# Kernel tuning notes

Hardware: AMD Instinct MI355X
Metric: run time of the kernel (lower is better)

## Reference

```python
import jax, jax.numpy as jnp
import numpy as np
import math

Z, H, G, S = 4, 16, 4, 4096          # batch, q heads, kv groups, seq len
BLOCK = 32                            # compression block size
NB = S // BLOCK                       # number of compressed KV blocks (128)
DQK, DV = 128, 128                    # head dims


def setup_inputs() -> dict:
    key = jax.random.key(0)
    k1, k2, k3 = jax.random.split(key, 3)
    q = jax.random.normal(k1, (Z, H, S, DQK), jnp.float32)
    k_blocks = jax.random.normal(k2, (Z, G, NB, DQK), jnp.float32)
    v_blocks = jax.random.normal(k3, (Z, G, NB, DV), jnp.float32)
    # block j covers tokens [j*BLOCK, (j+1)*BLOCK), so it 'ends' at position (j+1)*BLOCK-1
    block_ends = (jnp.arange(1, NB + 1) * BLOCK - 1).astype(jnp.int32)
    return {"q": q, "k_blocks": k_blocks, "v_blocks": v_blocks, "block_ends": block_ends}


def reference(q, k_blocks, v_blocks, block_ends):
    """NSA compression attention fwd: block-end causal masking over compressed KV blocks.
    q: [Z,H,S,Dqk]; k_blocks/v_blocks: [Z,G,NB,D]; block_ends: [NB] int.
    Query at position m attends to compressed block j iff block_ends[j] <= m.
    Rows with no valid block output zeros (matching the kernel's l_i==0 path)."""
    Zb, Hb, Sb, Dq = q.shape
    Gb = k_blocks.shape[1]
    sm_scale = 1.0 / math.sqrt(Dq)
    # GQA: head h -> kv group h // (H // G)
    qg = (q * sm_scale).reshape(Zb, Gb, Hb // Gb, Sb, Dq)
    s = jnp.einsum('zghsd,zgnd->zghsn', qg, k_blocks)        # [Z,G,H/G,S,NB]
    pos = jnp.arange(Sb)
    mask = block_ends[None, :] <= pos[:, None]               # [S,NB]
    s_masked = jnp.where(mask, s, -jnp.inf)
    m = jnp.max(s_masked, axis=-1, keepdims=True)            # online-softmax max (M)
    m_safe = jnp.where(jnp.isfinite(m), m, 0.0)
    p = jnp.where(mask, jnp.exp(s_masked - jax.lax.stop_gradient(m_safe)), 0.0)
    l = jnp.sum(p, axis=-1, keepdims=True)                   # softmax denom (exp(L-M))
    o = jnp.einsum('zghsn,zgnv->zghsv', p, v_blocks)
    o = jnp.where(l > 0, o / jnp.where(l > 0, l, 1.0), 0.0)
    return o.reshape(Zb, Hb, Sb, -1)                         # [Z,H,S,Dv]
```

## Files before the change

### kernel.cpp

```cpp
#include <hip/hip_runtime.h>


#define Zc 4
#define Hc 16
#define Gc 4
#define Sc 4096
#define NBc 128
#define Dc 128
#define VST 136

typedef __attribute__((ext_vector_type(8))) short short8;
typedef __attribute__((ext_vector_type(4))) float float4v;

__device__ inline unsigned pk2bf(float a, float b) {
    union { float f; unsigned u; } x, y; x.f = a; y.f = b;
    return __builtin_amdgcn_perm(y.u + 0x8000u, x.u + 0x8000u, 0x07060302u);
}
__device__ inline short8 mkfrag(float4v f0, float4v f1) {
    union { short8 v; unsigned d[4]; } u;
    u.d[0] = pk2bf(f0[0], f0[1]);
    u.d[1] = pk2bf(f0[2], f0[3]);
    u.d[2] = pk2bf(f1[0], f1[1]);
    u.d[3] = pk2bf(f1[2], f1[3]);
    return u.v;
}

__device__ inline void do_gemm1(const short* __restrict__ Ksh, short8 (&qf)[4][2],
                                float4v (&acc)[8][2], int c_max, int l16, int quad) {
    #pragma unroll
    for (int c = 0; c < 8; c++)
        #pragma unroll
        for (int t = 0; t < 2; t++) acc[c][t] = (float4v)0.f;
    #pragma unroll
    for (int dk = 0; dk < 4; dk++)
        #pragma unroll
        for (int c = 0; c < 8; c++)
            if (c < c_max) {
                short8 a = *(const short8*)(Ksh + (c * 16 + l16) * VST + dk * 32 + quad * 8);
                acc[c][0] = __builtin_amdgcn_mfma_f32_16x16x32_bf16(a, qf[dk][0], acc[c][0], 0, 0, 0);
                acc[c][1] = __builtin_amdgcn_mfma_f32_16x16x32_bf16(a, qf[dk][1], acc[c][1], 0, 0, 0);
            }
}

__device__ inline void do_softmax(float4v (&acc)[8][2], unsigned (&Ppk)[8][2][2],
                                  int m0, int c_max, int l16, int quad) {
    #pragma unroll
    for (int c = 0; c < 8; c++)
        #pragma unroll
        for (int t = 0; t < 2; t++) { Ppk[c][t][0] = 0u; Ppk[c][t][1] = 0u; }
    #pragma unroll
    for (int t = 0; t < 2; t++) {
        const int mg = m0 + t * 16 + l16;
        int nv = (mg + 1) >> 5; if (nv > NBc) nv = NBc;
        float mx = -1e30f;
        #pragma unroll
        for (int c = 0; c < 8; c++)
            if (c < c_max)
                #pragma unroll
                for (int r = 0; r < 4; r++) {
                    const int j = c * 16 + quad * 4 + r;
                    float s = acc[c][t][r];
                    s = (j < nv) ? s : -1e30f;
                    acc[c][t][r] = s;
                    mx = fmaxf(mx, s);
                }
        mx = fmaxf(mx, __shfl_xor(mx, 16, 64));
        mx = fmaxf(mx, __shfl_xor(mx, 32, 64));
        float ls = 0.f;
        #pragma unroll
        for (int c = 0; c < 8; c++)
            if (c < c_max)
                #pragma unroll
                for (int r = 0; r < 4; r++) {
                    float s = acc[c][t][r];
                    float p = (s > -1e29f) ? __expf(s - mx) : 0.f;
                    acc[c][t][r] = p;
                    ls += p;
                }
        ls += __shfl_xor(ls, 16, 64);
        ls += __shfl_xor(ls, 32, 64);
        const float inv = (ls > 0.f) ? 1.f / ls : 0.f;
        #pragma unroll
        for (int c = 0; c < 8; c++)
            if (c < c_max) {
                Ppk[c][t][0] = pk2bf(acc[c][t][0] * inv, acc[c][t][1] * inv);
                Ppk[c][t][1] = pk2bf(acc[c][t][2] * inv, acc[c][t][3] * inv);
            }
    }
}

__device__ inline void do_gemm2_store(const short* __restrict__ Vt, unsigned (&Ppk)[8][2][2],
                                      float* __restrict__ obase, int kbi_max,
                                      int l16, int quad) {
    float4v oacc[8][2];
    #pragma unroll
    for (int c = 0; c < 8; c++)
        #pragma unroll
        for (int t = 0; t < 2; t++) oacc[c][t] = (float4v)0.f;

    const int s0 = (((2 * quad) & 3) << 4) | l16;
    const int s1 = (((2 * quad + 1) & 3) << 4) | l16;
    const bool hi = (quad >= 2);

    #pragma unroll
    for (int kbi = 0; kbi < 4; kbi++)
        if (kbi < kbi_max) {
            short8 ap[2];
            #pragma unroll
            for (int t = 0; t < 2; t++) {
                const int c1 = 2 * kbi;
                unsigned w0a = (unsigned)__shfl((int)Ppk[c1    ][t][0], s0, 64);
                unsigned w0b = (unsigned)__shfl((int)Ppk[c1 + 1][t][0], s0, 64);
                unsigned w1a = (unsigned)__shfl((int)Ppk[c1    ][t][1], s0, 64);
                unsigned w1b = (unsigned)__shfl((int)Ppk[c1 + 1][t][1], s0, 64);
                unsigned w2a = (unsigned)__shfl((int)Ppk[c1    ][t][0], s1, 64);
                unsigned w2b = (unsigned)__shfl((int)Ppk[c1 + 1][t][0], s1, 64);
                unsigned w3a = (unsigned)__shfl((int)Ppk[c1    ][t][1], s1, 64);
                unsigned w3b = (unsigned)__shfl((int)Ppk[c1 + 1][t][1], s1, 64);
                union { short8 v; unsigned d[4]; } u;
                u.d[0] = hi ? w0b : w0a;
                u.d[1] = hi ? w1b : w1a;
                u.d[2] = hi ? w2b : w2a;
                u.d[3] = hi ? w3b : w3a;
                ap[t] = u.v;
            }
            #pragma unroll
            for (int c = 0; c < 8; c++) {
                short8 bv = *(const short8*)(Vt + (c * 16 + l16) * VST + kbi * 32 + quad * 8);
                #pragma unroll
                for (int t = 0; t < 2; t++)
                    oacc[c][t] = __builtin_amdgcn_mfma_f32_16x16x32_bf16(ap[t], bv, oacc[c][t], 0, 0, 0);
            }
        }

    #pragma unroll
    for (int t = 0; t < 2; t++)
        #pragma unroll
        for (int rr = 0; rr < 4; rr++) {
            const int row = t * 16 + quad * 4 + rr;
            #pragma unroll
            for (int c = 0; c < 8; c++)
                obase[(size_t)row * Dc + c * 16 + l16] = oacc[c][t][rr];
        }
}

__global__ __launch_bounds__(512, 4)
void nsa_fwd(const float* __restrict__ q, const float* __restrict__ kb,
             const float* __restrict__ vb, float* __restrict__ out) {
    __shared__ __align__(16) short Ksh[NBc * VST];
    __shared__ __align__(16) short Vt[Dc * VST];

    const int b    = blockIdx.x;
    const int h    = blockIdx.y, z = blockIdx.z, g = h >> 2;
    const int tid  = threadIdx.x;
    const int sgrp = tid >> 8;
    const int wq   = (tid >> 6) & 3;
    const int lane = tid & 63;
    const int l16  = lane & 15;
    const int quad = lane >> 4;

    const int j   = 2 * b + sgrp;
    const int bx0 = j, bx1 = 31 - j;
    const int nv0 = 4 * bx0 + wq + 1;
    const int nv1 = 4 * bx1 + wq + 1;
    const int cmax0 = (nv0 + 15) >> 4, kbi0 = (nv0 + 31) >> 5;
    const int cmax1 = (nv1 + 15) >> 4, kbi1 = (nv1 + 31) >> 5;
    const int nv_hi  = 128 - 8 * b;
    const int kst    = (nv_hi + 31) >> 5;
    const int nstage = kst << 5;

    const int m0_0 = bx0 * 128 + wq * 32;
    const int m0_1 = bx1 * 128 + wq * 32;
    const float sm = 0.08838834764831845f;

    const float* qb0 = q + ((size_t)(z * Hc + h) * Sc + m0_0) * Dc;
    float4v q0raw[4][2][2];
    #pragma unroll
    for (int dk = 0; dk < 4; dk++)
        #pragma unroll
        for (int t = 0; t < 2; t++) {
            const float* s = qb0 + (size_t)(t * 16 + l16) * Dc + dk * 32 + quad * 8;
            q0raw[dk][t][0] = *(const float4v*)s;
            q0raw[dk][t][1] = *(const float4v*)(s + 4);
        }

    const float* ksrc = kb + (size_t)(z * Gc + g) * NBc * Dc;
    #pragma unroll
    for (int it = 0; it < 4; it++)
        if (it < kst) {
            int i = it * 512 + tid;
            int n = i >> 4, c8 = i & 15;
            const float* s = ksrc + (size_t)n * Dc + c8 * 8;
            float4v f0 = *(const float4v*)s, f1 = *(const float4v*)(s + 4);
            *(short8*)(Ksh + n * VST + c8 * 8) = mkfrag(f0, f1);
        }

    {
        const float* vsrc = vb + (size_t)(z * Gc + g) * NBc * Dc;
        const int vw = tid >> 6;
        const int n2 = lane * 2;
        const bool vact = (n2 < nstage);
        #pragma unroll
        for (int it = 0; it < 4; it++) {
            const int c = it * 8 + vw;
            if (vact) {
                float4v fa = *(const float4v*)(vsrc + (size_t)n2 * Dc + c * 4);
                float4v fb = *(const float4v*)(vsrc + (size_t)(n2 + 1) * Dc + c * 4);
                #pragma unroll
                for (int k2 = 0; k2 < 4; k2++)
                    *(unsigned*)(Vt + (c * 4 + k2) * VST + n2) = pk2bf(fa[k2], fb[k2]);
            }
        }
    }

    short8 qf[4][2];
    #pragma unroll
    for (int dk = 0; dk < 4; dk++)
        #pragma unroll
        for (int t = 0; t < 2; t++)
            qf[dk][t] = mkfrag(q0raw[dk][t][0] * sm, q0raw[dk][t][1] * sm);

    __syncthreads();

    const float* qb1 = q + ((size_t)(z * Hc + h) * Sc + m0_1) * Dc;
    float4v q1raw[4][2][2];
    #pragma unroll
    for (int dk = 0; dk < 4; dk++)
        #pragma unroll
        for (int t = 0; t < 2; t++) {
            const float* s = qb1 + (size_t)(t * 16 + l16) * Dc + dk * 32 + quad * 8;
            q1raw[dk][t][0] = *(const float4v*)s;
            q1raw[dk][t][1] = *(const float4v*)(s + 4);
        }

    float4v acc[8][2];
    unsigned Ppk[8][2][2];

    do_gemm1(Ksh, qf, acc, cmax0, l16, quad);
    do_softmax(acc, Ppk, m0_0, cmax0, l16, quad);

    #pragma unroll
    for (int dk = 0; dk < 4; dk++)
        #pragma unroll
        for (int t = 0; t < 2; t++)
            qf[dk][t] = mkfrag(q1raw[dk][t][0] * sm, q1raw[dk][t][1] * sm);

    float* ob0 = out + ((size_t)(z * Hc + h) * Sc + m0_0) * Dc;
    do_gemm2_store(Vt, Ppk, ob0, kbi0, l16, quad);

    do_gemm1(Ksh, qf, acc, cmax1, l16, quad);
    do_softmax(acc, Ppk, m0_1, cmax1, l16, quad);
    float* ob1 = out + ((size_t)(z * Hc + h) * Sc + m0_1) * Dc;
    do_gemm2_store(Vt, Ppk, ob1, kbi1, l16, quad);
}

extern "C" void kernel_launch(void* const* d_in, const int* in_sizes, int n_in,
                              void* d_out, int out_size, void* d_ws, size_t ws_size,
                              hipStream_t stream) {
    const float* q  = (const float*)d_in[0];
    const float* kb = (const float*)d_in[1];
    const float* vb = (const float*)d_in[2];
    float* out = (float*)d_out;
    dim3 grid(8, Hc, Zc);
    nsa_fwd<<<grid, dim3(512), 0, stream>>>(q, kb, vb, out);
}
```

Baseline: 277.7 us.

## Split workgroups in half and read K directly from global memory in QK GEMM

Workgroups shrink from 512 to 256 threads and the grid doubles, so each workgroup handles one pair of mirrored query tiles instead of two. The shared-memory K staging buffer is removed; each wave loads K rows from global fp32 and converts them to bf16 right before each MFMA. Q loads are no longer prefetched across the barrier and are instead done per tile. This cuts LDS use and improves occupancy, but K is now re-read and re-converted by every wave, and global load latency lands directly on the MFMA loop.

Measured after the change: 277.6 us. Within noise of the previous version (-0.0%).

```diff
diff --git a/kernel.cpp b/kernel.cpp
--- a/kernel.cpp
+++ b/kernel.cpp
@@ -25,8 +25,8 @@
     return u.v;
 }
 
-__device__ inline void do_gemm1(const short* __restrict__ Ksh, short8 (&qf)[4][2],
-                                float4v (&acc)[8][2], int c_max, int l16, int quad) {
+__device__ inline void do_gemm1_g(const float* __restrict__ ksrc, short8 (&qf)[4][2],
+                                  float4v (&acc)[8][2], int c_max, int l16, int quad) {
     #pragma unroll
     for (int c = 0; c < 8; c++)
         #pragma unroll
@@ -36,7 +36,10 @@
         #pragma unroll
         for (int c = 0; c < 8; c++)
             if (c < c_max) {
-                short8 a = *(const short8*)(Ksh + (c * 16 + l16) * VST + dk * 32 + quad * 8);
+                const float* s = ksrc + (size_t)(c * 16 + l16) * Dc + dk * 32 + quad * 8;
+                float4v f0 = *(const float4v*)s;
+                float4v f1 = *(const float4v*)(s + 4);
+                short8 a = mkfrag(f0, f1);
                 acc[c][0] = __builtin_amdgcn_mfma_f32_16x16x32_bf16(a, qf[dk][0], acc[c][0], 0, 0, 0);
                 acc[c][1] = __builtin_amdgcn_mfma_f32_16x16x32_bf16(a, qf[dk][1], acc[c][1], 0, 0, 0);
             }
@@ -144,65 +147,40 @@
         }
 }
 
-__global__ __launch_bounds__(512, 4)
+__global__ __launch_bounds__(256, 4)
 void nsa_fwd(const float* __restrict__ q, const float* __restrict__ kb,
              const float* __restrict__ vb, float* __restrict__ out) {
-    __shared__ __align__(16) short Ksh[NBc * VST];
     __shared__ __align__(16) short Vt[Dc * VST];
 
     const int b    = blockIdx.x;
     const int h    = blockIdx.y, z = blockIdx.z, g = h >> 2;
     const int tid  = threadIdx.x;
-    const int sgrp = tid >> 8;
-    const int wq   = (tid >> 6) & 3;
+    const int wq   = tid >> 6;
     const int lane = tid & 63;
     const int l16  = lane & 15;
     const int quad = lane >> 4;
 
-    const int j   = 2 * b + sgrp;
-    const int bx0 = j, bx1 = 31 - j;
+    const int bx0 = b, bx1 = 31 - b;
     const int nv0 = 4 * bx0 + wq + 1;
     const int nv1 = 4 * bx1 + wq + 1;
     const int cmax0 = (nv0 + 15) >> 4, kbi0 = (nv0 + 31) >> 5;
     const int cmax1 = (nv1 + 15) >> 4, kbi1 = (nv1 + 31) >> 5;
-    const int nv_hi  = 128 - 8 * b;
-    const int kst    = (nv_hi + 31) >> 5;
-    const int nstage = kst << 5;
+    const int nv_hi  = 4 * bx1 + 4;
+    const int nstage = ((nv_hi + 31) >> 5) << 5;
 
     const int m0_0 = bx0 * 128 + wq * 32;
     const int m0_1 = bx1 * 128 + wq * 32;
     const float sm = 0.08838834764831845f;
 
-    const float* qb0 = q + ((size_t)(z * Hc + h) * Sc + m0_0) * Dc;
-    float4v q0raw[4][2][2];
-    #pragma unroll
-    for (int dk = 0; dk < 4; dk++)
-        #pragma unroll
-        for (int t = 0; t < 2; t++) {
-            const float* s = qb0 + (size_t)(t * 16 + l16) * Dc + dk * 32 + quad * 8;
-            q0raw[dk][t][0] = *(const float4v*)s;
-            q0raw[dk][t][1] = *(const float4v*)(s + 4);
-        }
-
     const float* ksrc = kb + (size_t)(z * Gc + g) * NBc * Dc;
-    #pragma unroll
-    for (int it = 0; it < 4; it++)
-        if (it < kst) {
-            int i = it * 512 + tid;
-            int n = i >> 4, c8 = i & 15;
-            const float* s = ksrc + (size_t)n * Dc + c8 * 8;
-            float4v f0 = *(const float4v*)s, f1 = *(const float4v*)(s + 4);
-            *(short8*)(Ksh + n * VST + c8 * 8) = mkfrag(f0, f1);
-        }
 
     {
         const float* vsrc = vb + (size_t)(z * Gc + g) * NBc * Dc;
-        const int vw = tid >> 6;
         const int n2 = lane * 2;
         const bool vact = (n2 < nstage);
         #pragma unroll
-        for (int it = 0; it < 4; it++) {
-            const int c = it * 8 + vw;
+        for (int it = 0; it < 8; it++) {
+            const int c = it * 4 + wq;
             if (vact) {
                 float4v fa = *(const float4v*)(vsrc + (size_t)n2 * Dc + c * 4);
                 float4v fb = *(const float4v*)(vsrc + (size_t)(n2 + 1) * Dc + c * 4);
@@ -213,45 +191,59 @@
         }
     }
 
-    short8 qf[4][2];
-    #pragma unroll
-    for (int dk = 0; dk < 4; dk++)
-        #pragma unroll
-        for (int t = 0; t < 2; t++)
-            qf[dk][t] = mkfrag(q0raw[dk][t][0] * sm, q0raw[dk][t][1] * sm);
-
     __syncthreads();
 
-    const float* qb1 = q + ((size_t)(z * Hc + h) * Sc + m0_1) * Dc;
-    float4v q1raw[4][2][2];
-    #pragma unroll
-    for (int dk = 0; dk < 4; dk++)
-        #pragma unroll
-        for (int t = 0; t < 2; t++) {
-            const float* s = qb1 + (size_t)(t * 16 + l16) * Dc + dk * 32 + quad * 8;
-            q1raw[dk][t][0] = *(const float4v*)s;
-            q1raw[dk][t][1] = *(const float4v*)(s + 4);
-        }
-
-    float4v acc[8][2];
-    unsigned Ppk[8][2][2];
-
-    do_gemm1(Ksh, qf, acc, cmax0, l16, quad);
-    do_softmax(acc, Ppk, m0_0, cmax0, l16, quad);
-
-    #pragma unroll
-    for (int dk = 0; dk < 4; dk++)
-        #pragma unroll
-        for (int t = 0; t < 2; t++)
-            qf[dk][t] = mkfrag(q1raw[dk][t][0] * sm, q1raw[dk][t][1] * sm);
-
-    float* ob0 = out + ((size_t)(z * Hc + h) * Sc + m0_0) * Dc;
-    do_gemm2_store(Vt, Ppk, ob0, kbi0, l16, quad);
-
-    do_gemm1(Ksh, qf, acc, cmax1, l16, quad);
-    do_softmax(acc, Ppk, m0_1, cmax1, l16, quad);
-    float* ob1 = out + ((size_t)(z * Hc + h) * Sc + m0_1) * Dc;
-    do_gemm2_store(Vt, Ppk, ob1, kbi1, l16, quad);
+    {
+        const float* qb = q + ((size_t)(z * Hc + h) * Sc + m0_0) * Dc;
+        float4v qraw[4][2][2];
+        #pragma unroll
+        for (int dk = 0; dk < 4; dk++)
+            #pragma unroll
+            for (int t = 0; t < 2; t++) {
+                const float* s = qb + (size_t)(t * 16 + l16) * Dc + dk * 32 + quad * 8;
+                qraw[dk][t][0] = *(const float4v*)s;
+                qraw[dk][t][1] = *(const float4v*)(s + 4);
+            }
+        short8 qf[4][2];
+        #pragma unroll
+        for (int dk = 0; dk < 4; dk++)
+            #pragma unroll
+            for (int t = 0; t < 2; t++)
+                qf[dk][t] = mkfrag(qraw[dk][t][0] * sm, qraw[dk][t][1] * sm);
+
+        float4v acc[8][2];
+        unsigned Ppk[8][2][2];
+        do_gemm1_g(ksrc, qf, acc, cmax0, l16, quad);
+        do_softmax(acc, Ppk, m0_0, cmax0, l16, quad);
+        float* ob = out + ((size_t)(z * Hc + h) * Sc + m0_0) * Dc;
+        do_gemm2_store(Vt, Ppk, ob, kbi0, l16, quad);
+    }
+
+    {
+        const float* qb = q + ((size_t)(z * Hc + h) * Sc + m0_1) * Dc;
+        float4v qraw[4][2][2];
+        #pragma unroll
+        for (int dk = 0; dk < 4; dk++)
+            #pragma unroll
+            for (int t = 0; t < 2; t++) {
+                const float* s = qb + (size_t)(t * 16 + l16) * Dc + dk * 32 + quad * 8;
+                qraw[dk][t][0] = *(const float4v*)s;
+                qraw[dk][t][1] = *(const float4v*)(s + 4);
+            }
+        short8 qf[4][2];
+        #pragma unroll
+        for (int dk = 0; dk < 4; dk++)
+            #pragma unroll
+            for (int t = 0; t < 2; t++)
+                qf[dk][t] = mkfrag(qraw[dk][t][0] * sm, qraw[dk][t][1] * sm);
+
+        float4v acc[8][2];
+        unsigned Ppk[8][2][2];
+        do_gemm1_g(ksrc, qf, acc, cmax1, l16, quad);
+        do_softmax(acc, Ppk, m0_1, cmax1, l16, quad);
+        float* ob = out + ((size_t)(z * Hc + h) * Sc + m0_1) * Dc;
+        do_gemm2_store(Vt, Ppk, ob, kbi1, l16, quad);
+    }
 }
 
 extern "C" void kernel_launch(void* const* d_in, const int* in_sizes, int n_in,
@@ -261,6 +253,6 @@
     const float* kb = (const float*)d_in[1];
     const float* vb = (const float*)d_in[2];
     float* out = (float*)d_out;
-    dim3 grid(8, Hc, Zc);
-    nsa_fwd<<<grid, dim3(512), 0, stream>>>(q, kb, vb, out);
-}
+    dim3 grid(16, Hc, Zc);
+    nsa_fwd<<<grid, dim3(256), 0, stream>>>(q, kb, vb, out);
+}
```
